# Kernel optimization log

Hardware: AMD Instinct MI355X
Metric: run time of the kernel (lower is better)

## Reference

```python
import jax, jax.numpy as jnp
import numpy as np

TOKENS, HIDDEN, N_EXPERTS = 16384, 2048, 64
JITTER_EPS = 0.01
Z_LOSS_COEFF = 0.001


def setup_inputs() -> dict:
    key = jax.random.key(0)
    k1, k2 = jax.random.split(key)
    x = jax.random.normal(k1, (TOKENS, HIDDEN), dtype=jnp.float32)
    w = jax.random.normal(k2, (N_EXPERTS, HIDDEN), dtype=jnp.float32) * 0.02  # router weight [E,H]
    return {"x": x, "w": w}


def _route_pass(scores_sel, scores, jitter_eps):
    # scores_sel: logits possibly with -inf at already-selected expert (top-2 pass)
    # scores:     original logits (used for abs/clamp factor, as in torch code)
    mx = jnp.max(scores_sel, axis=-1, keepdims=True)                      # [N,1]
    factor = jnp.maximum(jnp.abs(scores), mx)                             # scores.abs().clamp(min=mx)
    mask = jax.lax.stop_gradient((mx - scores) / factor > 2.0 * jitter_eps)
    masked_logits = jnp.where(mask, -jnp.inf, scores_sel)
    # eval path (training=False): selected_experts = argmax of (masked-for-selection) scores
    sel = jnp.argmax(scores_sel, axis=-1)[..., None]                      # [N,1] int
    gates = jax.nn.softmax(masked_logits, axis=-1)
    # mask_for_one: selected == argmax(gates) holds deterministically in eval -> 1.0
    mult = jnp.take_along_axis(gates, sel, axis=-1)                       # [N,1]
    return mult, sel


def reference(x, w):
    logits = x @ w.T                                                      # [N,E]
    # z-loss (identity on logits in forward; scalar returned for completeness)
    z_loss = Z_LOSS_COEFF * jnp.mean(jnp.square(jax.nn.logsumexp(logits, axis=-1)))
    original_gates = jax.nn.softmax(logits, axis=-1)
    # top-1 pass
    m1, s1 = _route_pass(logits, logits, JITTER_EPS)
    # top-2 pass: mask out the first selection
    e_idx = jnp.arange(logits.shape[-1])[None, :]
    scores2 = jnp.where(e_idx == s1, -jnp.inf, logits)
    m2, s2 = _route_pass(scores2, logits, JITTER_EPS)
    multiplier = jnp.concatenate([m1, m2], axis=-1)                       # [N,2]
    selected_experts = jnp.concatenate([s1, s2], axis=-1)                 # [N,2]
    return multiplier, original_gates, selected_experts, z_loss
```

## Files before the change

### kernel.cpp

```cpp
#include <hip/hip_runtime.h>
#include <math.h>

#define TOKENS 16384
#define HIDDEN 2048
#define NEXP   64
#define MT     16
#define NBLK   (TOKENS / MT)
#define BK     256
#define NCH    (HIDDEN / BK)
#define CB     16384

#define GATES_OFF (TOKENS * 2)
#define SEL_OFF   (GATES_OFF + TOKENS * NEXP)
#define Z_OFF     (SEL_OFF + TOKENS * 2)

#define WIMG_BYTES (NEXP * HIDDEN * 2 * 2)

typedef __attribute__((ext_vector_type(8))) _Float16 f16x8;
typedef __attribute__((ext_vector_type(4))) float    f32x4;

__device__ __forceinline__ float wave_sum64(float v) {
    #pragma unroll
    for (int s = 1; s < 64; s <<= 1) v += __shfl_xor(v, s, 64);
    return v;
}

__device__ __forceinline__ void dma16(const void* g, void* l) {
    __builtin_amdgcn_global_load_lds(
        (const __attribute__((address_space(1))) unsigned int*)g,
        (__attribute__((address_space(3))) unsigned int*)l, 16, 0, 0);
}

__global__ __launch_bounds__(256) void wconvert(
    const float* __restrict__ w, uint4* __restrict__ wimg)
{
    const int s = blockIdx.x * 256 + threadIdx.x;
    const int c    = s >> 10;
    const int r    = s & 1023;
    const int l    = r & 63;
    const int nt   = (r >> 6) & 1;
    const int kh   = (r >> 7) & 1;
    const int term = (r >> 8) & 1;
    const int eh   = (r >> 9) & 1;
    const int e = eh * 32 + nt * 16 + (l & 15);
    const int k = c * 64 + kh * 32 + (l >> 4) * 8;

    const float* src = w + (size_t)e * HIDDEN + k;
    union { _Float16 f[8]; uint4 u; } o;
    #pragma unroll
    for (int j = 0; j < 8; ++j) {
        const float v = src[j];
        const _Float16 h = (_Float16)v;
        o.f[j] = (term == 0) ? h : (_Float16)((v - (float)h) * 4096.f);
    }
    wimg[s] = o.u;
}

__device__ __forceinline__ void cvt_split(const float4 a, const float4 b,
                                          f16x8& hi, f16x8& lo) {
    union { _Float16 f[8]; f16x8 v; } H, L;
    #pragma unroll
    for (int j = 0; j < 4; ++j) {
        const float s0 = (&a.x)[j];
        const float s1 = (&b.x)[j];
        const _Float16 h0 = (_Float16)s0;
        const _Float16 h1 = (_Float16)s1;
        H.f[j]     = h0;
        H.f[j + 4] = h1;
        L.f[j]     = (_Float16)((s0 - (float)h0) * 4096.f);
        L.f[j + 4] = (_Float16)((s1 - (float)h1) * 4096.f);
    }
    hi = H.v; lo = L.v;
}

__global__ __launch_bounds__(64) void router_main(
    const float* __restrict__ x, const uint4* __restrict__ wimg,
    float* __restrict__ out, float* __restrict__ zpartial)
{
    __shared__ __align__(16) unsigned char smem[2 * CB];

    const int lane = threadIdx.x & 63;
    const int t0   = blockIdx.x * MT;
    const int rowr = lane & 15;
    const int kg   = lane >> 4;

    const float* xq = x + (size_t)(t0 + rowr) * HIDDEN + kg * 4;

    f32x4 acc0[4], acc1[4];
    #pragma unroll
    for (int g = 0; g < 4; ++g) { acc0[g] = (f32x4)0.f; acc1[g] = (f32x4)0.f; }

    #pragma unroll
    for (int j = 0; j < 16; ++j)
        dma16(xq + j * 16, smem + j * 1024);

    for (int c = 0; c < NCH; ++c) {
        asm volatile("s_waitcnt vmcnt(0)" ::: "memory");
        __builtin_amdgcn_sched_barrier(0);

        if (c + 1 < NCH) {
            const float* sg = xq + (c + 1) * BK;
            unsigned char* dg = smem + ((c + 1) & 1) * CB;
            #pragma unroll
            for (int j = 0; j < 16; ++j)
                dma16(sg + j * 16, dg + j * 1024);
        }

        const unsigned char* ab = smem + (c & 1) * CB + kg * 512 + rowr * 16;
        const uint4* wc0 = wimg + (size_t)c * 4096 + lane;
        #pragma unroll
        for (int s = 0; s < 8; ++s) {
            const uint4* p = wc0 + (s >> 1) * 1024 + (s & 1) * 128;
            f16x8 bh[4], bl[4];
            bh[0] = *(const f16x8*)(p);
            bh[1] = *(const f16x8*)(p + 64);
            bh[2] = *(const f16x8*)(p + 512);
            bh[3] = *(const f16x8*)(p + 576);
            bl[0] = *(const f16x8*)(p + 256);
            bl[1] = *(const f16x8*)(p + 320);
            bl[2] = *(const f16x8*)(p + 768);
            bl[3] = *(const f16x8*)(p + 832);

            const float4 va = *(const float4*)(ab + s * 2048);
            const float4 vb = *(const float4*)(ab + s * 2048 + 256);
            f16x8 Ah, Al;
            cvt_split(va, vb, Ah, Al);
            #pragma unroll
            for (int g = 0; g < 4; ++g) {
                acc0[g] = __builtin_amdgcn_mfma_f32_16x16x32_f16(Ah, bh[g], acc0[g], 0, 0, 0);
                acc1[g] = __builtin_amdgcn_mfma_f32_16x16x32_f16(Ah, bl[g], acc1[g], 0, 0, 0);
                acc1[g] = __builtin_amdgcn_mfma_f32_16x16x32_f16(Al, bh[g], acc1[g], 0, 0, 0);
            }
        }
    }

    float zsum = 0.f;
    #pragma unroll
    for (int r = 0; r < 4; ++r) {
        const int t = kg * 4 + r;
        float v[4]; int e[4];
        #pragma unroll
        for (int g = 0; g < 4; ++g) {
            v[g] = acc0[g][r] + acc1[g][r] * (1.f / 4096.f);
            e[g] = g * 16 + rowr;
        }

        float bv = v[0]; int bi = e[0];
        #pragma unroll
        for (int g = 1; g < 4; ++g)
            if (v[g] > bv) { bv = v[g]; bi = e[g]; }
        #pragma unroll
        for (int st = 1; st < 16; st <<= 1) {
            const float ov = __shfl_xor(bv, st, 64);
            const int   oi = __shfl_xor(bi, st, 64);
            if (ov > bv || (ov == bv && oi < bi)) { bv = ov; bi = oi; }
        }
        const float max1 = bv; const int s1 = bi;

        float e1[4], se = 0.f, sm1 = 0.f;
        #pragma unroll
        for (int g = 0; g < 4; ++g) {
            e1[g] = expf(v[g] - max1);
            se += e1[g];
            const bool m1 = (max1 - v[g]) > 0.02f * fmaxf(fabsf(v[g]), max1);
            sm1 += m1 ? 0.f : e1[g];
        }
        #pragma unroll
        for (int st = 1; st < 16; st <<= 1) {
            se  += __shfl_xor(se, st, 64);
            sm1 += __shfl_xor(sm1, st, 64);
        }

        #pragma unroll
        for (int g = 0; g < 4; ++g)
            out[GATES_OFF + (size_t)(t0 + t) * NEXP + e[g]] = e1[g] / se;

        const float lse = max1 + logf(se);
        if (rowr == 0) zsum += lse * lse;

        float bv2 = (e[0] == s1) ? -INFINITY : v[0]; int bi2 = e[0];
        #pragma unroll
        for (int g = 1; g < 4; ++g) {
            const float cv = (e[g] == s1) ? -INFINITY : v[g];
            if (cv > bv2) { bv2 = cv; bi2 = e[g]; }
        }
        #pragma unroll
        for (int st = 1; st < 16; st <<= 1) {
            const float ov = __shfl_xor(bv2, st, 64);
            const int   oi = __shfl_xor(bi2, st, 64);
            if (ov > bv2 || (ov == bv2 && oi < bi2)) { bv2 = ov; bi2 = oi; }
        }
        const float max2 = bv2; const int s2 = bi2;

        float sm2 = 0.f;
        #pragma unroll
        for (int g = 0; g < 4; ++g) {
            const bool m2 = (max2 - v[g]) > 0.02f * fmaxf(fabsf(v[g]), max2);
            sm2 += (m2 || e[g] == s1) ? 0.f : expf(v[g] - max2);
        }
        #pragma unroll
        for (int st = 1; st < 16; st <<= 1)
            sm2 += __shfl_xor(sm2, st, 64);

        if (rowr == 0) {
            const size_t trow = (size_t)(t0 + t) * 2;
            out[trow + 0] = 1.f / sm1;
            out[trow + 1] = 1.f / sm2;
            out[SEL_OFF + trow + 0] = (float)s1;
            out[SEL_OFF + trow + 1] = (float)s2;
        }
    }

    const float zt = wave_sum64(zsum);
    if (lane == 0) zpartial[blockIdx.x] = zt;
}

__global__ __launch_bounds__(256) void zfinal(
    const float* __restrict__ zpartial, float* __restrict__ out)
{
    const int tid = threadIdx.x;
    float v = zpartial[tid] + zpartial[tid + 256]
            + zpartial[tid + 512] + zpartial[tid + 768];
    v = wave_sum64(v);
    __shared__ float red[4];
    if ((tid & 63) == 0) red[tid >> 6] = v;
    __syncthreads();
    if (tid == 0) {
        const float tot = red[0] + red[1] + red[2] + red[3];
        out[Z_OFF] = 0.001f * (tot / (float)TOKENS);
    }
}

extern "C" void kernel_launch(void* const* d_in, const int* in_sizes, int n_in,
                              void* d_out, int out_size, void* d_ws, size_t ws_size,
                              hipStream_t stream) {
    const float* x = (const float*)d_in[0];
    const float* w = (const float*)d_in[1];
    float* out = (float*)d_out;

    uint4* wimg     = (uint4*)d_ws;
    float* zpartial = (float*)((char*)d_ws + WIMG_BYTES);

    wconvert<<<128, 256, 0, stream>>>(w, wimg);
    router_main<<<NBLK, 64, 0, stream>>>(x, wimg, out, zpartial);
    zfinal<<<1, 256, 0, stream>>>(zpartial, out);
}
```

Baseline: 236.2 us.

## Share staged weight chunks in LDS across four waves per block

Each block now handles 64 tokens with four waves instead of 16 tokens with one wave. Each K-chunk of the split-fp16 weight image is DMA'd into LDS once and shared by all four waves, rather than every wave reading the weights from global/L2. This cuts redundant weight traffic. It adds a block-wide barrier per chunk and a double-buffered 128KB LDS footprint, which limits the launch to one block of four waves per CU. The z-loss partials are reduced inside the block, and the final kernel is adjusted to the new partial count.

```diff
diff --git a/kernel.cpp b/kernel.cpp
--- a/kernel.cpp
+++ b/kernel.cpp
@@ -4,11 +4,12 @@
 #define TOKENS 16384
 #define HIDDEN 2048
 #define NEXP   64
-#define MT     16
+#define MT     64
 #define NBLK   (TOKENS / MT)
-#define BK     256
-#define NCH    (HIDDEN / BK)
-#define CB     16384
+#define CK     128
+#define NCH    (HIDDEN / CK)
+#define XCB    8192
+#define BUFB   65536
 
 #define GATES_OFF (TOKENS * 2)
 #define SEL_OFF   (GATES_OFF + TOKENS * NEXP)
@@ -73,56 +74,75 @@
     hi = H.v; lo = L.v;
 }
 
-__global__ __launch_bounds__(64) void router_main(
+__global__ __launch_bounds__(256, 1) void router_main(
     const float* __restrict__ x, const uint4* __restrict__ wimg,
     float* __restrict__ out, float* __restrict__ zpartial)
 {
-    __shared__ __align__(16) unsigned char smem[2 * CB];
-
-    const int lane = threadIdx.x & 63;
-    const int t0   = blockIdx.x * MT;
+    __shared__ __align__(16) unsigned char smem[2 * BUFB];
+    __shared__ float zred[4];
+
+    const int tid  = threadIdx.x;
+    const int wv   = __builtin_amdgcn_readfirstlane(tid >> 6);
+    const int lane = tid & 63;
     const int rowr = lane & 15;
     const int kg   = lane >> 4;
-
-    const float* xq = x + (size_t)(t0 + rowr) * HIDDEN + kg * 4;
+    const int t0b  = blockIdx.x * MT;
+
+    const float* xq = x + (size_t)(t0b + wv * 16 + rowr) * HIDDEN + kg * 4;
+    const uint4* wB = wimg + lane;
 
     f32x4 acc0[4], acc1[4];
     #pragma unroll
     for (int g = 0; g < 4; ++g) { acc0[g] = (f32x4)0.f; acc1[g] = (f32x4)0.f; }
 
-    #pragma unroll
-    for (int j = 0; j < 16; ++j)
-        dma16(xq + j * 16, smem + j * 1024);
-
+    {
+        unsigned char* xd = smem + wv * XCB;
+        #pragma unroll
+        for (int j = 0; j < 8; ++j)
+            dma16(xq + j * 16, xd + j * 1024);
+        unsigned char* bd = smem + 32768;
+        #pragma unroll
+        for (int i = 0; i < 8; ++i) {
+            const int m = wv * 8 + i;
+            dma16(wB + m * 64, bd + m * 1024);
+        }
+    }
+    __syncthreads();
+
+    #pragma unroll 2
     for (int c = 0; c < NCH; ++c) {
-        asm volatile("s_waitcnt vmcnt(0)" ::: "memory");
-        __builtin_amdgcn_sched_barrier(0);
+        const int buf = c & 1;
 
         if (c + 1 < NCH) {
-            const float* sg = xq + (c + 1) * BK;
-            unsigned char* dg = smem + ((c + 1) & 1) * CB;
+            unsigned char* xd = smem + (buf ^ 1) * BUFB + wv * XCB;
             #pragma unroll
-            for (int j = 0; j < 16; ++j)
-                dma16(sg + j * 16, dg + j * 1024);
-        }
-
-        const unsigned char* ab = smem + (c & 1) * CB + kg * 512 + rowr * 16;
-        const uint4* wc0 = wimg + (size_t)c * 4096 + lane;
-        #pragma unroll
-        for (int s = 0; s < 8; ++s) {
-            const uint4* p = wc0 + (s >> 1) * 1024 + (s & 1) * 128;
+            for (int j = 0; j < 8; ++j)
+                dma16(xq + (c + 1) * CK + j * 16, xd + j * 1024);
+            unsigned char* bd = smem + (buf ^ 1) * BUFB + 32768;
+            #pragma unroll
+            for (int i = 0; i < 8; ++i) {
+                const int m = wv * 8 + i;
+                dma16(wB + (size_t)(c + 1) * 2048 + m * 64, bd + m * 1024);
+            }
+        }
+
+        const unsigned char* xb = smem + buf * BUFB + wv * XCB + kg * 512 + rowr * 16;
+        const unsigned char* bb = smem + buf * BUFB + 32768;
+        #pragma unroll
+        for (int s = 0; s < 4; ++s) {
+            const int pb = ((s >> 1) * 1024 + (s & 1) * 128 + lane) * 16;
             f16x8 bh[4], bl[4];
-            bh[0] = *(const f16x8*)(p);
-            bh[1] = *(const f16x8*)(p + 64);
-            bh[2] = *(const f16x8*)(p + 512);
-            bh[3] = *(const f16x8*)(p + 576);
-            bl[0] = *(const f16x8*)(p + 256);
-            bl[1] = *(const f16x8*)(p + 320);
-            bl[2] = *(const f16x8*)(p + 768);
-            bl[3] = *(const f16x8*)(p + 832);
-
-            const float4 va = *(const float4*)(ab + s * 2048);
-            const float4 vb = *(const float4*)(ab + s * 2048 + 256);
+            bh[0] = *(const f16x8*)(bb + pb);
+            bh[1] = *(const f16x8*)(bb + pb + 64 * 16);
+            bh[2] = *(const f16x8*)(bb + pb + 512 * 16);
+            bh[3] = *(const f16x8*)(bb + pb + 576 * 16);
+            bl[0] = *(const f16x8*)(bb + pb + 256 * 16);
+            bl[1] = *(const f16x8*)(bb + pb + 320 * 16);
+            bl[2] = *(const f16x8*)(bb + pb + 768 * 16);
+            bl[3] = *(const f16x8*)(bb + pb + 832 * 16);
+
+            const float4 va = *(const float4*)(xb + s * 2048);
+            const float4 vb = *(const float4*)(xb + s * 2048 + 256);
             f16x8 Ah, Al;
             cvt_split(va, vb, Ah, Al);
             #pragma unroll
@@ -132,12 +152,14 @@
                 acc1[g] = __builtin_amdgcn_mfma_f32_16x16x32_f16(Al, bh[g], acc1[g], 0, 0, 0);
             }
         }
+
+        __syncthreads();
     }
 
     float zsum = 0.f;
     #pragma unroll
     for (int r = 0; r < 4; ++r) {
-        const int t = kg * 4 + r;
+        const int t = wv * 16 + kg * 4 + r;
         float v[4]; int e[4];
         #pragma unroll
         for (int g = 0; g < 4; ++g) {
@@ -173,7 +195,7 @@
 
         #pragma unroll
         for (int g = 0; g < 4; ++g)
-            out[GATES_OFF + (size_t)(t0 + t) * NEXP + e[g]] = e1[g] / se;
+            out[GATES_OFF + (size_t)(t0b + t) * NEXP + e[g]] = e1[g] / se;
 
         const float lse = max1 + logf(se);
         if (rowr == 0) zsum += lse * lse;
@@ -203,7 +225,7 @@
             sm2 += __shfl_xor(sm2, st, 64);
 
         if (rowr == 0) {
-            const size_t trow = (size_t)(t0 + t) * 2;
+            const size_t trow = (size_t)(t0b + t) * 2;
             out[trow + 0] = 1.f / sm1;
             out[trow + 1] = 1.f / sm2;
             out[SEL_OFF + trow + 0] = (float)s1;
@@ -212,15 +234,17 @@
     }
 
     const float zt = wave_sum64(zsum);
-    if (lane == 0) zpartial[blockIdx.x] = zt;
+    if (lane == 0) zred[wv] = zt;
+    __syncthreads();
+    if (tid == 0)
+        zpartial[blockIdx.x] = zred[0] + zred[1] + zred[2] + zred[3];
 }
 
 __global__ __launch_bounds__(256) void zfinal(
     const float* __restrict__ zpartial, float* __restrict__ out)
 {
     const int tid = threadIdx.x;
-    float v = zpartial[tid] + zpartial[tid + 256]
-            + zpartial[tid + 512] + zpartial[tid + 768];
+    float v = zpartial[tid];
     v = wave_sum64(v);
     __shared__ float red[4];
     if ((tid & 63) == 0) red[tid >> 6] = v;
@@ -242,6 +266,6 @@
     float* zpartial = (float*)((char*)d_ws + WIMG_BYTES);
 
     wconvert<<<128, 256, 0, stream>>>(w, wimg);
-    router_main<<<NBLK, 64, 0, stream>>>(x, wimg, out, zpartial);
+    router_main<<<NBLK, 256, 0, stream>>>(x, wimg, out, zpartial);
     zfinal<<<1, 256, 0, stream>>>(zpartial, out);
 }
```

After: 221.6 us. -6.2%, faster.
